# Optimization experiments

Measured on AMD Instinct MI355X. Metric: run time of the kernel, lower is better.

## Reference

```python
import jax, jax.numpy as jnp
import numpy as np

NUM_GRAPHS = 512
NODES_PER_GRAPH = 30
IN_CH = 8
HID = 64
NUM_LAYERS = 5
BRANCHES = 41
BN_EPS = 1e-5


def setup_inputs() -> dict:
    key = jax.random.key(0)
    ks = jax.random.split(key, 16)
    N = NUM_GRAPHS * NODES_PER_GRAPH
    x = jax.random.normal(ks[0], (N, IN_CH), jnp.float32)
    branch_u = jax.random.randint(ks[1], (BRANCHES,), 0, NODES_PER_GRAPH, jnp.int32)
    branch_v = jax.random.randint(ks[2], (BRANCHES,), 0, NODES_PER_GRAPH, jnp.int32)
    # Build bidirectional edge_index from the per-graph branch list + graph offsets
    offsets = (jnp.arange(NUM_GRAPHS, dtype=jnp.int32) * NODES_PER_GRAPH)
    u = (branch_u[None, :] + offsets[:, None]).reshape(-1)
    v = (branch_v[None, :] + offsets[:, None]).reshape(-1)
    edge_index = jnp.stack([jnp.concatenate([u, v]), jnp.concatenate([v, u])], axis=0)  # [2, E]
    s = 0.05
    inp = {
        'x': x, 'edge_index': edge_index, 'branch_u': branch_u, 'branch_v': branch_v,
        'num_graphs': NUM_GRAPHS,
        'Wp': jax.random.normal(ks[3], (IN_CH, HID), jnp.float32) * s,
        'bp': jnp.zeros((HID,), jnp.float32),
        'W1': jax.random.normal(ks[4], (NUM_LAYERS, 2 * HID, 32), jnp.float32) * s,
        'b1': jnp.zeros((NUM_LAYERS, 32), jnp.float32),
        'W2': jax.random.normal(ks[5], (NUM_LAYERS, 32, HID * HID), jnp.float32) * s,
        'b2': jnp.zeros((NUM_LAYERS, HID * HID), jnp.float32),
        'Wr': jax.random.normal(ks[6], (NUM_LAYERS, HID, HID), jnp.float32) * s,
        'br': jnp.zeros((NUM_LAYERS, HID), jnp.float32),
        'gamma': jnp.ones((NUM_LAYERS, HID), jnp.float32),
        'beta': jnp.zeros((NUM_LAYERS, HID), jnp.float32),
        'rmean': jax.random.normal(ks[7], (NUM_LAYERS, HID), jnp.float32) * s,
        'rvar': jax.random.uniform(ks[8], (NUM_LAYERS, HID), jnp.float32) + 0.5,
        'Wm1': jax.random.normal(ks[9], (2 * HID, HID), jnp.float32) * s,
        'bm1': jnp.zeros((HID,), jnp.float32),
        'Wm2': jax.random.normal(ks[10], (HID, 1), jnp.float32) * s,
        'bm2': jnp.zeros((1,), jnp.float32),
    }
    return inp


def reference(x, edge_index, branch_u, branch_v, num_graphs,
              Wp, bp, W1, b1, W2, b2, Wr, br,
              gamma, beta, rmean, rvar, Wm1, bm1, Wm2, bm2):
    N = x.shape[0]
    src, dst = edge_index[0], edge_index[1]  # messages flow src -> dst
    h = x @ Wp + bp  # [N, H]
    # in-degree for mean aggregation (clamped to avoid div-by-zero on isolated nodes)
    deg = jax.ops.segment_sum(jnp.ones(src.shape, h.dtype), dst, num_segments=N)
    deg = jnp.maximum(deg, 1.0)[:, None]
    for l in range(NUM_LAYERS):
        res = h
        ea = jnp.concatenate([h[src], h[dst]], axis=-1)              # [E, 2H] edge_attr
        w = jax.nn.relu(ea @ W1[l] + b1[l]) @ W2[l] + b2[l]          # [E, H*H]
        w = w.reshape(-1, HID, HID)                                  # [E, in, out]
        msg = jnp.einsum('eh,eho->eo', h[src], w)                    # gather + bmm
        agg = jax.ops.segment_sum(msg, dst, num_segments=N) / deg    # scatter-mean
        h2 = agg + h @ Wr[l] + br[l]                                 # NNConv root weight + bias
        # BatchNorm1d (eval mode: running stats)
        h2 = (h2 - rmean[l]) * (gamma[l] / jnp.sqrt(rvar[l] + BN_EPS)) + beta[l]
        h = jax.nn.relu(h2) + res                                    # dropout off (eval) + residual
    offsets = jnp.arange(num_graphs, dtype=src.dtype) * NODES_PER_GRAPH
    u_idx = (branch_u[None, :] + offsets[:, None]).reshape(-1)
    v_idx = (branch_v[None, :] + offsets[:, None]).reshape(-1)
    ef = jnp.concatenate([h[u_idx], h[v_idx]], axis=-1)              # [G*41, 2H]
    out = jax.nn.relu(ef @ Wm1 + bm1) @ Wm2 + bm2                    # [G*41, 1]
    return out
```

## Files before the change

kernel.cpp:

```cpp
#include <hip/hip_runtime.h>


typedef float f32x4 __attribute__((ext_vector_type(4)));
typedef _Float16 f16x8 __attribute__((ext_vector_type(8)));

#define MFMA16(a, b, c) __builtin_amdgcn_mfma_f32_16x16x32_f16((a), (b), (c), 0, 0, 0)

#define WS_W2S 0u
#define WS_W1S 1351680u
#define WS_WRS 1392640u
#define WS_BNS 1433600u
#define WS_BNH 1434880u
#define WS_WM1H 1436160u
#define WS_WM1L 1452544u

__device__ inline f16x8 ld_frag_g(const _Float16* p) {
  union { uint4 u; f16x8 f; } c;
  c.u = *(const uint4*)p;
  return c.f;
}
__device__ inline f16x8 ld_frag_s(const _Float16* p) { return *(const f16x8*)p; }

__global__ __launch_bounds__(256) void prep_kernel(
    const float* __restrict__ W1, const float* __restrict__ W2,
    const float* __restrict__ b2, const float* __restrict__ Wr,
    const float* __restrict__ gamma, const float* __restrict__ beta,
    const float* __restrict__ rmean, const float* __restrict__ rvar,
    const float* __restrict__ Wm1, unsigned char* __restrict__ ws) {
  __shared__ __align__(16) float tile[32][68];
  const int tid = threadIdx.x;
  if (blockIdx.x < 330) {
    int l = blockIdx.x / 66, jb = blockIdx.x % 66;
    int s = tid >> 3, n0 = (tid & 7) * 8;
    int j = jb * 32 + s;
    const float* srcp = (j < 2048)
        ? (W2 + (size_t)l * 131072 + (size_t)j * 64 + n0)
        : (b2 + (size_t)l * 4096 + (size_t)(j - 2048) * 64 + n0);
    *(f32x4*)&tile[s][n0] = *(const f32x4*)srcp;
    *(f32x4*)&tile[s][n0 + 4] = *(const f32x4*)(srcp + 4);
    __syncthreads();
    int n = tid >> 2, sb = (tid & 3) * 8;
    f16x8 hv;
#pragma unroll
    for (int u = 0; u < 8; ++u) hv[u] = (_Float16)tile[sb + u][n];
    _Float16* dst = (_Float16*)(ws + WS_W2S) +
                    (size_t)l * 135168 + (size_t)jb * 2048 + n * 32 + sb;
    *(f16x8*)dst = hv;
    return;
  }
  int idx = (blockIdx.x - 330) * 256 + tid;
  _Float16* W1s = (_Float16*)(ws + WS_W1S);
  _Float16* Wrs = (_Float16*)(ws + WS_WRS);
  float* bns = (float*)(ws + WS_BNS);
  float* bnh = (float*)(ws + WS_BNH);
  _Float16* Wm1h = (_Float16*)(ws + WS_WM1H);
  _Float16* Wm1l = (_Float16*)(ws + WS_WM1L);
  if (idx < 20480) {
    int l = idx / 4096, r = idx % 4096;
    int t = r >> 10, n = (r >> 5) & 31, s2 = r & 31;
    int j = t * 32 + s2;
    W1s[idx] = (_Float16)W1[l * 4096 + j * 32 + n];
  } else if (idx < 40960) {
    int i3 = idx - 20480;
    int l = i3 / 4096, r = i3 % 4096;
    int t = r >> 11, rem = r & 2047;
    int n = rem >> 5, s2 = rem & 31;
    int j = t * 32 + s2;
    Wrs[i3] = (_Float16)Wr[l * 4096 + j * 64 + n];
  } else if (idx < 41280) {
    int i4 = idx - 40960;
    float sc = gamma[i4] * rsqrtf(rvar[i4] + 1e-5f);
    bns[i4] = sc;
    bnh[i4] = beta[i4] - rmean[i4] * sc;
  } else if (idx < 49472) {
    int i5 = idx - 41280;
    int t = i5 >> 11, n = (i5 >> 5) & 63, s2 = i5 & 31;
    float w = Wm1[(t * 32 + s2) * 64 + n];
    _Float16 hi = (_Float16)w;
    Wm1h[i5] = hi;
    Wm1l[i5] = (_Float16)(w - (float)hi);
  }
}

__global__ __launch_bounds__(512, 4) void gnn_kernel(
    const float* __restrict__ x, const int* __restrict__ bu, const int* __restrict__ bv,
    const float* __restrict__ Wp, const float* __restrict__ bp,
    const float* __restrict__ b1, const float* __restrict__ brr,
    const float* __restrict__ bm1, const float* __restrict__ Wm2,
    const float* __restrict__ bm2,
    const _Float16* __restrict__ W2s, const _Float16* __restrict__ W1s,
    const _Float16* __restrict__ Wrs, const _Float16* __restrict__ Wm1h,
    const _Float16* __restrict__ Wm1l,
    const float* __restrict__ bns, const float* __restrict__ bnh,
    float* __restrict__ out) {
  __shared__ __align__(16) float hF[32][68];
  __shared__ __align__(16) _Float16 hH[32][72];
  __shared__ __align__(16) _Float16 hL[32][72];
  __shared__ __align__(16) float zE[96][36];
  __shared__ __align__(16) float agg[32][68];
  __shared__ int srcn[96], dstn[96];
  __shared__ float invdeg[32];

  const int tid = threadIdx.x;
  const int g = blockIdx.x;
  const int wv = tid >> 6;
  const int ln = tid & 63;
  const int q = ln >> 4;
  const int m16 = ln & 15;
  const f32x4 zero4 = {0.f, 0.f, 0.f, 0.f};
  float* const hidT = &zE[0][0];

  if (tid < 96) {
    int s, d;
    if (tid < 41)      { s = bu[tid];      d = bv[tid]; }
    else if (tid < 82) { s = bv[tid - 41]; d = bu[tid - 41]; }
    else               { s = 0;            d = 0; }
    srcn[tid] = s; dstn[tid] = d;
  }
  if (tid < 136) { hF[30 + tid / 68][tid % 68] = 0.f; }
  if (tid < 144) {
    hH[30 + tid / 72][tid % 72] = (_Float16)0.f;
    hL[30 + tid / 72][tid % 72] = (_Float16)0.f;
  }
  for (int u = tid; u < 32 * 68; u += 512) ((float*)agg)[u] = 0.f;
  __syncthreads();
  if (tid < 32) {
    int cnt = 0;
    for (int e = 0; e < 82; ++e) cnt += (dstn[e] == tid) ? 1 : 0;
    invdeg[tid] = 1.0f / (float)(cnt > 0 ? cnt : 1);
  }
  for (int u = tid; u < 30 * 64; u += 512) {
    int n = u >> 6, c = u & 63;
    float acc = bp[c];
#pragma unroll
    for (int k = 0; k < 8; ++k) acc += x[(g * 30 + n) * 8 + k] * Wp[k * 64 + c];
    hF[n][c] = acc;
    _Float16 hi = (_Float16)acc;
    hH[n][c] = hi;
    hL[n][c] = (_Float16)(acc - (float)hi);
  }
  __syncthreads();

  for (int l = 0; l < 5; ++l) {
    const int ncolR = (wv & 3) * 16 + m16;
    const int mtR = wv >> 2;
    float scl = bns[l * 64 + ncolR];
    float sft = bnh[l * 64 + ncolR];
    float brb = brr[l * 64 + ncolR];
    f32x4 racc = zero4;
    {
      f16x8 wb0 = ld_frag_g(Wrs + ((l * 2 + 0) * 64 + ncolR) * 32 + q * 8);
      f16x8 wb1 = ld_frag_g(Wrs + ((l * 2 + 1) * 64 + ncolR) * 32 + q * 8);
      racc = MFMA16(ld_frag_s(&hH[mtR * 16 + m16][q * 8]), wb0, racc);
      racc = MFMA16(ld_frag_s(&hH[mtR * 16 + m16][32 + q * 8]), wb1, racc);
      racc = MFMA16(ld_frag_s(&hL[mtR * 16 + m16][q * 8]), wb0, racc);
      racc = MFMA16(ld_frag_s(&hL[mtR * 16 + m16][32 + q * 8]), wb1, racc);
    }
    {
      int ntz = wv & 1, g2 = wv >> 1;
      int ncol = ntz * 16 + m16;
      f16x8 bf[4];
#pragma unroll
      for (int t = 0; t < 4; ++t)
        bf[t] = ld_frag_g(W1s + ((l * 4 + t) * 32 + ncol) * 32 + q * 8);
      float b1v = b1[l * 32 + ncol];
#pragma unroll
      for (int mi = 0; mi < 2; ++mi) {
        int mt = g2 + mi * 4;
        if (mt < 6) {
          int e = mt * 16 + m16;
          int sn = srcn[e], dn = dstn[e];
          f32x4 acc = zero4;
#pragma unroll
          for (int t = 0; t < 4; ++t) {
            int nd = (t < 2) ? sn : dn;
            acc = MFMA16(ld_frag_s(&hH[nd][(t & 1) * 32 + q * 8]), bf[t], acc);
          }
#pragma unroll
          for (int t = 0; t < 4; ++t) {
            int nd = (t < 2) ? sn : dn;
            acc = MFMA16(ld_frag_s(&hL[nd][(t & 1) * 32 + q * 8]), bf[t], acc);
          }
#pragma unroll
          for (int r = 0; r < 4; ++r) {
            int e2 = mt * 16 + q * 4 + r;
            zE[e2][ncol] = fmaxf(acc[r] + b1v, 0.f);
          }
        }
      }
    }
    __syncthreads();

    {
      int nt = wv & 3, mh = wv >> 2;
      int e0 = mh * 48 + m16, e1 = e0 + 16, e2 = e0 + 32;
      f16x8 hA[3][2];
      {
        int s0 = srcn[e0], s1 = srcn[e1], s2 = srcn[e2];
        hA[0][0] = ld_frag_s(&hH[s0][q * 8]); hA[0][1] = ld_frag_s(&hH[s0][32 + q * 8]);
        hA[1][0] = ld_frag_s(&hH[s1][q * 8]); hA[1][1] = ld_frag_s(&hH[s1][32 + q * 8]);
        hA[2][0] = ld_frag_s(&hH[s2][q * 8]); hA[2][1] = ld_frag_s(&hH[s2][32 + q * 8]);
      }
      f32x4 macc[3] = {zero4, zero4, zero4};
      const _Float16* Wb = W2s + (size_t)l * 135168 + (nt * 16 + m16) * 32 + q * 8;
      f16x8 r0a = ld_frag_g(Wb + (size_t)0 * 2048), r0b = ld_frag_g(Wb + (size_t)1 * 2048);
      f16x8 r1a = ld_frag_g(Wb + (size_t)2 * 2048), r1b = ld_frag_g(Wb + (size_t)3 * 2048);
      f16x8 r2a = ld_frag_g(Wb + (size_t)4 * 2048), r2b = ld_frag_g(Wb + (size_t)5 * 2048);
      f16x8 r3a, r3b;
      f16x8 Bz0 = ld_frag_g(Wb + (size_t)64 * 2048), Bz1 = ld_frag_g(Wb + (size_t)65 * 2048);
      macc[0] = MFMA16(hA[0][0], Bz0, macc[0]); macc[0] = MFMA16(hA[0][1], Bz1, macc[0]);
      macc[1] = MFMA16(hA[1][0], Bz0, macc[1]); macc[1] = MFMA16(hA[1][1], Bz1, macc[1]);
      macc[2] = MFMA16(hA[2][0], Bz0, macc[2]); macc[2] = MFMA16(hA[2][1], Bz1, macc[2]);
      for (int cb = 0; cb < 32; cb += 4) {
        f32x4 zb0 = *(const f32x4*)&zE[e0][cb];
        f32x4 zb1 = *(const f32x4*)&zE[e1][cb];
        f32x4 zb2 = *(const f32x4*)&zE[e2][cb];
        {
          r3a = ld_frag_g(Wb + (size_t)(2 * cb + 6) * 2048);
          r3b = ld_frag_g(Wb + (size_t)(2 * cb + 7) * 2048);
          _Float16 z0 = (_Float16)zb0[0], z1 = (_Float16)zb1[0], z2 = (_Float16)zb2[0];
          macc[0] = MFMA16(hA[0][0] * z0, r0a, macc[0]); macc[0] = MFMA16(hA[0][1] * z0, r0b, macc[0]);
          macc[1] = MFMA16(hA[1][0] * z1, r0a, macc[1]); macc[1] = MFMA16(hA[1][1] * z1, r0b, macc[1]);
          macc[2] = MFMA16(hA[2][0] * z2, r0a, macc[2]); macc[2] = MFMA16(hA[2][1] * z2, r0b, macc[2]);
        }
        {
          r0a = ld_frag_g(Wb + (size_t)(2 * cb + 8) * 2048);
          r0b = ld_frag_g(Wb + (size_t)(2 * cb + 9) * 2048);
          _Float16 z0 = (_Float16)zb0[1], z1 = (_Float16)zb1[1], z2 = (_Float16)zb2[1];
          macc[0] = MFMA16(hA[0][0] * z0, r1a, macc[0]); macc[0] = MFMA16(hA[0][1] * z0, r1b, macc[0]);
          macc[1] = MFMA16(hA[1][0] * z1, r1a, macc[1]); macc[1] = MFMA16(hA[1][1] * z1, r1b, macc[1]);
          macc[2] = MFMA16(hA[2][0] * z2, r1a, macc[2]); macc[2] = MFMA16(hA[2][1] * z2, r1b, macc[2]);
        }
        {
          r1a = ld_frag_g(Wb + (size_t)(2 * cb + 10) * 2048);
          r1b = ld_frag_g(Wb + (size_t)(2 * cb + 11) * 2048);
          _Float16 z0 = (_Float16)zb0[2], z1 = (_Float16)zb1[2], z2 = (_Float16)zb2[2];
          macc[0] = MFMA16(hA[0][0] * z0, r2a, macc[0]); macc[0] = MFMA16(hA[0][1] * z0, r2b, macc[0]);
          macc[1] = MFMA16(hA[1][0] * z1, r2a, macc[1]); macc[1] = MFMA16(hA[1][1] * z1, r2b, macc[1]);
          macc[2] = MFMA16(hA[2][0] * z2, r2a, macc[2]); macc[2] = MFMA16(hA[2][1] * z2, r2b, macc[2]);
        }
        {
          r2a = ld_frag_g(Wb + (size_t)(2 * cb + 12) * 2048);
          r2b = ld_frag_g(Wb + (size_t)(2 * cb + 13) * 2048);
          _Float16 z0 = (_Float16)zb0[3], z1 = (_Float16)zb1[3], z2 = (_Float16)zb2[3];
          macc[0] = MFMA16(hA[0][0] * z0, r3a, macc[0]); macc[0] = MFMA16(hA[0][1] * z0, r3b, macc[0]);
          macc[1] = MFMA16(hA[1][0] * z1, r3a, macc[1]); macc[1] = MFMA16(hA[1][1] * z1, r3b, macc[1]);
          macc[2] = MFMA16(hA[2][0] * z2, r3a, macc[2]); macc[2] = MFMA16(hA[2][1] * z2, r3b, macc[2]);
        }
      }
#pragma unroll
      for (int mi = 0; mi < 3; ++mi) {
#pragma unroll
        for (int r = 0; r < 4; ++r) {
          int e = mh * 48 + mi * 16 + q * 4 + r;
          if (e < 82) atomicAdd(&agg[dstn[e]][nt * 16 + m16], macc[mi][r]);
        }
      }
    }
    __syncthreads();

    {
#pragma unroll
      for (int r = 0; r < 4; ++r) {
        int row = mtR * 16 + q * 4 + r;
        if (row < 30) {
          float v = agg[row][ncolR] * invdeg[row] + racc[r] + brb;
          agg[row][ncolR] = 0.f;
          v = v * scl + sft;
          float hn = fmaxf(v, 0.f) + hF[row][ncolR];
          hF[row][ncolR] = hn;
          _Float16 hi = (_Float16)hn;
          hH[row][ncolR] = hi;
          hL[row][ncolR] = (_Float16)(hn - (float)hi);
        }
      }
    }
    __syncthreads();
  }

  {
    int nt = wv & 3, mtb = wv >> 2;
    int c = nt * 16 + m16;
    float bm1v = bm1[c];
    int nmt = (mtb == 0) ? 2 : 1;
    for (int p2 = 0; p2 < nmt; ++p2) {
      int mt = (p2 == 0) ? mtb : 2;
      int e = mt * 16 + m16;
      int un = srcn[e], vn = dstn[e];
      f32x4 acc = zero4;
#pragma unroll
      for (int t = 0; t < 4; ++t) {
        int nd = (t < 2) ? un : vn;
        int co = (t & 1) * 32 + q * 8;
        f16x8 bh2 = ld_frag_g(Wm1h + (t * 64 + c) * 32 + q * 8);
        f16x8 bl2 = ld_frag_g(Wm1l + (t * 64 + c) * 32 + q * 8);
        f16x8 ah = ld_frag_s(&hH[nd][co]);
        f16x8 al = ld_frag_s(&hL[nd][co]);
        acc = MFMA16(ah, bh2, acc);
        acc = MFMA16(al, bh2, acc);
        acc = MFMA16(ah, bl2, acc);
      }
      f32x4 res;
#pragma unroll
      for (int r = 0; r < 4; ++r) res[r] = fmaxf(acc[r] + bm1v, 0.f);
      *(f32x4*)&hidT[c * 48 + mt * 16 + (q << 2)] = res;
    }
  }
  __syncthreads();
  if (tid < 41) {
    float acc = bm2[0];
#pragma unroll 4
    for (int c = 0; c < 64; ++c) acc += hidT[c * 48 + tid] * Wm2[c];
    out[g * 41 + tid] = acc;
  }
}

extern "C" void kernel_launch(void* const* d_in, const int* in_sizes, int n_in,
                              void* d_out, int out_size, void* d_ws, size_t ws_size,
                              hipStream_t stream) {
  const float* x   = (const float*)d_in[0];
  const int* bu    = (const int*)d_in[2];
  const int* bv    = (const int*)d_in[3];
  const float* Wp  = (const float*)d_in[5];
  const float* bp  = (const float*)d_in[6];
  const float* W1  = (const float*)d_in[7];
  const float* b1  = (const float*)d_in[8];
  const float* W2  = (const float*)d_in[9];
  const float* b2  = (const float*)d_in[10];
  const float* Wr  = (const float*)d_in[11];
  const float* br  = (const float*)d_in[12];
  const float* gm  = (const float*)d_in[13];
  const float* bt  = (const float*)d_in[14];
  const float* rm  = (const float*)d_in[15];
  const float* rv  = (const float*)d_in[16];
  const float* Wm1 = (const float*)d_in[17];
  const float* bm1 = (const float*)d_in[18];
  const float* Wm2 = (const float*)d_in[19];
  const float* bm2 = (const float*)d_in[20];
  unsigned char* ws = (unsigned char*)d_ws;
  float* out = (float*)d_out;

  prep_kernel<<<524, 256, 0, stream>>>(W1, W2, b2, Wr, gm, bt, rm, rv, Wm1, ws);
  gnn_kernel<<<512, 512, 0, stream>>>(
      x, bu, bv, Wp, bp, b1, br, bm1, Wm2, bm2,
      (const _Float16*)(ws + WS_W2S),
      (const _Float16*)(ws + WS_W1S),
      (const _Float16*)(ws + WS_WRS),
      (const _Float16*)(ws + WS_WM1H),
      (const _Float16*)(ws + WS_WM1L),
      (const float*)(ws + WS_BNS),
      (const float*)(ws + WS_BNH),
      out);
}
```

Measured before the change: 229.6 us.

## Double block size and split edge-network K loop across two wave groups

Doubles the work-group to 1024 threads (16 waves) and splits the per-edge weight contraction over the 32 hidden channels into two halves, one per wave group, with both halves accumulating into shared agg via atomics. The root-weight MFMA and the BN/residual update move to waves 8-15, while the edge-MLP and final-MLP stages are spread one tile per wave to drop per-wave loops. The aim is more wave-level parallelism and latency hiding per graph. The cost is doubled atomic traffic on agg, tighter register limits from the 1024/8 launch bounds with possible spills, and fewer resident blocks per CU.

```diff
diff --git a/kernel.cpp b/kernel.cpp
--- a/kernel.cpp
+++ b/kernel.cpp
@@ -82,7 +82,7 @@
   }
 }
 
-__global__ __launch_bounds__(512, 4) void gnn_kernel(
+__global__ __launch_bounds__(1024, 8) void gnn_kernel(
     const float* __restrict__ x, const int* __restrict__ bu, const int* __restrict__ bv,
     const float* __restrict__ Wp, const float* __restrict__ bp,
     const float* __restrict__ b1, const float* __restrict__ brr,
@@ -108,6 +108,7 @@
   const int q = ln >> 4;
   const int m16 = ln & 15;
   const f32x4 zero4 = {0.f, 0.f, 0.f, 0.f};
+  const bool rootw = (wv >= 8);
   float* const hidT = &zE[0][0];
 
   if (tid < 96) {
@@ -122,14 +123,14 @@
     hH[30 + tid / 72][tid % 72] = (_Float16)0.f;
     hL[30 + tid / 72][tid % 72] = (_Float16)0.f;
   }
-  for (int u = tid; u < 32 * 68; u += 512) ((float*)agg)[u] = 0.f;
+  for (int u = tid; u < 32 * 68; u += 1024) ((float*)agg)[u] = 0.f;
   __syncthreads();
   if (tid < 32) {
     int cnt = 0;
     for (int e = 0; e < 82; ++e) cnt += (dstn[e] == tid) ? 1 : 0;
     invdeg[tid] = 1.0f / (float)(cnt > 0 ? cnt : 1);
   }
-  for (int u = tid; u < 30 * 64; u += 512) {
+  for (int u = tid; u < 30 * 64; u += 1024) {
     int n = u >> 6, c = u & 63;
     float acc = bp[c];
 #pragma unroll
@@ -143,12 +144,13 @@
 
   for (int l = 0; l < 5; ++l) {
     const int ncolR = (wv & 3) * 16 + m16;
-    const int mtR = wv >> 2;
-    float scl = bns[l * 64 + ncolR];
-    float sft = bnh[l * 64 + ncolR];
-    float brb = brr[l * 64 + ncolR];
+    const int mtR = (wv >> 2) & 1;
+    float scl = 0.f, sft = 0.f, brb = 0.f;
     f32x4 racc = zero4;
-    {
+    if (rootw) {
+      scl = bns[l * 64 + ncolR];
+      sft = bnh[l * 64 + ncolR];
+      brb = brr[l * 64 + ncolR];
       f16x8 wb0 = ld_frag_g(Wrs + ((l * 2 + 0) * 64 + ncolR) * 32 + q * 8);
       f16x8 wb1 = ld_frag_g(Wrs + ((l * 2 + 1) * 64 + ncolR) * 32 + q * 8);
       racc = MFMA16(ld_frag_s(&hH[mtR * 16 + m16][q * 8]), wb0, racc);
@@ -156,43 +158,37 @@
       racc = MFMA16(ld_frag_s(&hL[mtR * 16 + m16][q * 8]), wb0, racc);
       racc = MFMA16(ld_frag_s(&hL[mtR * 16 + m16][32 + q * 8]), wb1, racc);
     }
-    {
-      int ntz = wv & 1, g2 = wv >> 1;
+    if (wv < 12) {
+      int ntz = wv & 1, mt = wv >> 1;
       int ncol = ntz * 16 + m16;
       f16x8 bf[4];
 #pragma unroll
       for (int t = 0; t < 4; ++t)
         bf[t] = ld_frag_g(W1s + ((l * 4 + t) * 32 + ncol) * 32 + q * 8);
       float b1v = b1[l * 32 + ncol];
-#pragma unroll
-      for (int mi = 0; mi < 2; ++mi) {
-        int mt = g2 + mi * 4;
-        if (mt < 6) {
-          int e = mt * 16 + m16;
-          int sn = srcn[e], dn = dstn[e];
-          f32x4 acc = zero4;
-#pragma unroll
-          for (int t = 0; t < 4; ++t) {
-            int nd = (t < 2) ? sn : dn;
-            acc = MFMA16(ld_frag_s(&hH[nd][(t & 1) * 32 + q * 8]), bf[t], acc);
-          }
-#pragma unroll
-          for (int t = 0; t < 4; ++t) {
-            int nd = (t < 2) ? sn : dn;
-            acc = MFMA16(ld_frag_s(&hL[nd][(t & 1) * 32 + q * 8]), bf[t], acc);
-          }
-#pragma unroll
-          for (int r = 0; r < 4; ++r) {
-            int e2 = mt * 16 + q * 4 + r;
-            zE[e2][ncol] = fmaxf(acc[r] + b1v, 0.f);
-          }
-        }
+      int e = mt * 16 + m16;
+      int sn = srcn[e], dn = dstn[e];
+      f32x4 acc = zero4;
+#pragma unroll
+      for (int t = 0; t < 4; ++t) {
+        int nd = (t < 2) ? sn : dn;
+        acc = MFMA16(ld_frag_s(&hH[nd][(t & 1) * 32 + q * 8]), bf[t], acc);
+      }
+#pragma unroll
+      for (int t = 0; t < 4; ++t) {
+        int nd = (t < 2) ? sn : dn;
+        acc = MFMA16(ld_frag_s(&hL[nd][(t & 1) * 32 + q * 8]), bf[t], acc);
+      }
+#pragma unroll
+      for (int r = 0; r < 4; ++r) {
+        int e2 = mt * 16 + q * 4 + r;
+        zE[e2][ncol] = fmaxf(acc[r] + b1v, 0.f);
       }
     }
     __syncthreads();
 
     {
-      int nt = wv & 3, mh = wv >> 2;
+      int nt = wv & 3, mh = (wv >> 2) & 1, kh = wv >> 3;
       int e0 = mh * 48 + m16, e1 = e0 + 16, e2 = e0 + 32;
       f16x8 hA[3][2];
       {
@@ -203,15 +199,18 @@
       }
       f32x4 macc[3] = {zero4, zero4, zero4};
       const _Float16* Wb = W2s + (size_t)l * 135168 + (nt * 16 + m16) * 32 + q * 8;
-      f16x8 r0a = ld_frag_g(Wb + (size_t)0 * 2048), r0b = ld_frag_g(Wb + (size_t)1 * 2048);
-      f16x8 r1a = ld_frag_g(Wb + (size_t)2 * 2048), r1b = ld_frag_g(Wb + (size_t)3 * 2048);
-      f16x8 r2a = ld_frag_g(Wb + (size_t)4 * 2048), r2b = ld_frag_g(Wb + (size_t)5 * 2048);
+      const int c0 = kh * 16;
+      f16x8 r0a = ld_frag_g(Wb + (size_t)(2 * c0 + 0) * 2048), r0b = ld_frag_g(Wb + (size_t)(2 * c0 + 1) * 2048);
+      f16x8 r1a = ld_frag_g(Wb + (size_t)(2 * c0 + 2) * 2048), r1b = ld_frag_g(Wb + (size_t)(2 * c0 + 3) * 2048);
+      f16x8 r2a = ld_frag_g(Wb + (size_t)(2 * c0 + 4) * 2048), r2b = ld_frag_g(Wb + (size_t)(2 * c0 + 5) * 2048);
       f16x8 r3a, r3b;
-      f16x8 Bz0 = ld_frag_g(Wb + (size_t)64 * 2048), Bz1 = ld_frag_g(Wb + (size_t)65 * 2048);
-      macc[0] = MFMA16(hA[0][0], Bz0, macc[0]); macc[0] = MFMA16(hA[0][1], Bz1, macc[0]);
-      macc[1] = MFMA16(hA[1][0], Bz0, macc[1]); macc[1] = MFMA16(hA[1][1], Bz1, macc[1]);
-      macc[2] = MFMA16(hA[2][0], Bz0, macc[2]); macc[2] = MFMA16(hA[2][1], Bz1, macc[2]);
-      for (int cb = 0; cb < 32; cb += 4) {
+      if (kh == 0) {
+        f16x8 Bz0 = ld_frag_g(Wb + (size_t)64 * 2048), Bz1 = ld_frag_g(Wb + (size_t)65 * 2048);
+        macc[0] = MFMA16(hA[0][0], Bz0, macc[0]); macc[0] = MFMA16(hA[0][1], Bz1, macc[0]);
+        macc[1] = MFMA16(hA[1][0], Bz0, macc[1]); macc[1] = MFMA16(hA[1][1], Bz1, macc[1]);
+        macc[2] = MFMA16(hA[2][0], Bz0, macc[2]); macc[2] = MFMA16(hA[2][1], Bz1, macc[2]);
+      }
+      for (int cb = c0; cb < c0 + 16; cb += 4) {
         f32x4 zb0 = *(const f32x4*)&zE[e0][cb];
         f32x4 zb1 = *(const f32x4*)&zE[e1][cb];
         f32x4 zb2 = *(const f32x4*)&zE[e2][cb];
@@ -259,7 +258,7 @@
     }
     __syncthreads();
 
-    {
+    if (rootw) {
 #pragma unroll
       for (int r = 0; r < 4; ++r) {
         int row = mtR * 16 + q * 4 + r;
@@ -278,33 +277,29 @@
     __syncthreads();
   }
 
-  {
-    int nt = wv & 3, mtb = wv >> 2;
+  if (wv < 12) {
+    int nt = wv & 3, mt = wv >> 2;
     int c = nt * 16 + m16;
     float bm1v = bm1[c];
-    int nmt = (mtb == 0) ? 2 : 1;
-    for (int p2 = 0; p2 < nmt; ++p2) {
-      int mt = (p2 == 0) ? mtb : 2;
-      int e = mt * 16 + m16;
-      int un = srcn[e], vn = dstn[e];
-      f32x4 acc = zero4;
-#pragma unroll
-      for (int t = 0; t < 4; ++t) {
-        int nd = (t < 2) ? un : vn;
-        int co = (t & 1) * 32 + q * 8;
-        f16x8 bh2 = ld_frag_g(Wm1h + (t * 64 + c) * 32 + q * 8);
-        f16x8 bl2 = ld_frag_g(Wm1l + (t * 64 + c) * 32 + q * 8);
-        f16x8 ah = ld_frag_s(&hH[nd][co]);
-        f16x8 al = ld_frag_s(&hL[nd][co]);
-        acc = MFMA16(ah, bh2, acc);
-        acc = MFMA16(al, bh2, acc);
-        acc = MFMA16(ah, bl2, acc);
-      }
-      f32x4 res;
-#pragma unroll
-      for (int r = 0; r < 4; ++r) res[r] = fmaxf(acc[r] + bm1v, 0.f);
-      *(f32x4*)&hidT[c * 48 + mt * 16 + (q << 2)] = res;
-    }
+    int e = mt * 16 + m16;
+    int un = srcn[e], vn = dstn[e];
+    f32x4 acc = zero4;
+#pragma unroll
+    for (int t = 0; t < 4; ++t) {
+      int nd = (t < 2) ? un : vn;
+      int co = (t & 1) * 32 + q * 8;
+      f16x8 bh2 = ld_frag_g(Wm1h + (t * 64 + c) * 32 + q * 8);
+      f16x8 bl2 = ld_frag_g(Wm1l + (t * 64 + c) * 32 + q * 8);
+      f16x8 ah = ld_frag_s(&hH[nd][co]);
+      f16x8 al = ld_frag_s(&hL[nd][co]);
+      acc = MFMA16(ah, bh2, acc);
+      acc = MFMA16(al, bh2, acc);
+      acc = MFMA16(ah, bl2, acc);
+    }
+    f32x4 res;
+#pragma unroll
+    for (int r = 0; r < 4; ++r) res[r] = fmaxf(acc[r] + bm1v, 0.f);
+    *(f32x4*)&hidT[c * 48 + mt * 16 + (q << 2)] = res;
   }
   __syncthreads();
   if (tid < 41) {
@@ -341,7 +336,7 @@
   float* out = (float*)d_out;
 
   prep_kernel<<<524, 256, 0, stream>>>(W1, W2, b2, Wr, gm, bt, rm, rv, Wm1, ws);
-  gnn_kernel<<<512, 512, 0, stream>>>(
+  gnn_kernel<<<512, 1024, 0, stream>>>(
       x, bu, bv, Wp, bp, b1, br, bm1, Wm2, bm2,
       (const _Float16*)(ws + WS_W2S),
       (const _Float16*)(ws + WS_W1S),
```

New measurement: 453.7 us. +97.6%, slower.
